# Kernel tuning notes

Hardware: AMD Instinct MI355X
Metric: run time of the kernel (lower is better)

The kernel has to match this reference:

```python
import jax, jax.numpy as jnp
import numpy as np

B = 4      # cfg.TRAIN.IMS_PER_BATCH
P = 256    # proposals per image (equal per image; all labels > 0)
C = 151    # cfg.MODEL.NUM_CLASSES
R = 51     # cfg.MODEL.NUM_RELATIONS
W = 0.5    # cfg.REL_INFER.NONE_BGREL_WEIGHT


def setup_inputs() -> dict:
    key = jax.random.key(0)
    k1, k2, k3, k4 = jax.random.split(key, 4)
    roi_scores = jax.random.normal(k1, (B * P, C), dtype=jnp.float32)
    rel_scores = jax.random.normal(k2, (B * P * P, R), dtype=jnp.float32)
    roi_labels = jax.random.randint(k3, (B * P,), 1, C, dtype=jnp.int32)  # labels > 0 (fg only)
    # sparse relation co-occurrence matrix densified; background relation slice set to 1
    relationship_mat = (jax.random.uniform(k4, (C, C, R)) < 0.05).astype(jnp.float32)
    relationship_mat = relationship_mat.at[:, :, 0].set(1.0)
    return {
        "roi_scores": roi_scores,
        "rel_scores": rel_scores,
        "relationship_mat": relationship_mat,
        "roi_labels": roi_labels,
        "num_images": B,
    }


def reference(roi_scores, rel_scores, relationship_mat, roi_labels, num_images):
    nb = num_images
    p = roi_scores.shape[0] // nb
    rel = rel_scores.reshape(nb, p, p, -1)          # [B, P, P, R]
    labels = roi_labels.reshape(nb, p)              # [B, P]
    # computed in the original forward but unused by the returned loss
    _unary = jax.nn.log_softmax(roi_scores, axis=1)
    off_diag = (1.0 - jnp.eye(p, dtype=roi_scores.dtype))  # zero out p == q pairs

    def per_image(lab, rl):
        # lab: [P] int, rl: [P, P, R]
        A = relationship_mat[lab]        # [P, C, R]  rows gathered by subject label
        At = relationship_mat[:, lab]    # [C, P, R]  cols gathered by subject label
        # b[p,q,c] = A[p,c,0]*rl[p,q,0] + W * sum_{r>=1} A[p,c,r]*rl[p,q,r]
        b = A[:, None, :, 0] * rl[:, :, None, 0] \
            + W * jnp.einsum('pcr,pqr->pqc', A[..., 1:], rl[..., 1:])
        # t[p,q,c] = At[c,p,0]*rl[q,p,0] + W * sum_{r>=1} At[c,p,r]*rl[q,p,r]
        t = At[..., 0].T[:, None, :] * rl[..., 0].T[:, :, None] \
            + W * jnp.einsum('cpr,qpr->pqc', At[..., 1:], rl[..., 1:])
        theta = 0.5 * (b + t) * off_diag[:, :, None]  # mask diagonal pairs
        theta = theta.sum(0)                          # sum over partner p -> [P, C]
        logp = jax.nn.log_softmax(theta, axis=1)
        return -logp[jnp.arange(p), lab]              # [P]

    loss = jax.vmap(per_image)(labels, rel)           # [B, P]
    return loss.mean()
```

## Files before the change

kernel.cpp:

```cpp
#include <hip/hip_runtime.h>
#include <math.h>

#define NB 4
#define PP 256
#define CC 151
#define RR 51
#define CM 160
#define KI 64
#define KS 64
#define NROW (NB*PP)
#define RELTOT (NB*PP*PP*RR)
#define ALIM (RELTOT - 8)
#define MLB 10240

typedef _Float16 half8 __attribute__((ext_vector_type(8)));
typedef float floatx16 __attribute__((ext_vector_type(16)));

#define OFF_M1 ((size_t)0)
#define OFF_M2 (OFF_M1 + (size_t)CC*MLB*2)
#define OFF_PT (OFF_M2 + (size_t)CC*MLB*2)

__global__ __launch_bounds__(256) void prep_kernel(const float* __restrict__ M,
                                                   _Float16* __restrict__ m1,
                                                   _Float16* __restrict__ m2,
                                                   float* __restrict__ out) {
    const int l = blockIdx.x;
    const int mat = blockIdx.y;
    if (l == 0 && mat == 0 && threadIdx.x == 0) *out = 0.f;
    _Float16* dst = (mat ? m2 : m1) + (size_t)l * MLB;
    for (int e = threadIdx.x; e < MLB; e += 256) {
        int oct = e / 1280;
        int rem = e - oct * 1280;
        int c = rem >> 3, j = rem & 7;
        int r = oct * 8 + j;
        float v = 0.f;
        if (r < RR && c < CC) {
            size_t src = ((size_t)(mat ? c * CC + l : l * CC + c)) * RR + r;
            v = (r == 0 ? 0.5f : 0.25f) * M[src];
        }
        dst[e] = (_Float16)v;
    }
}

__global__ __launch_bounds__(256) void gemm_kernel(const float* __restrict__ rel,
                                                   const _Float16* __restrict__ m1,
                                                   const _Float16* __restrict__ m2,
                                                   const int* __restrict__ labels,
                                                   float* __restrict__ part) {
    __shared__ _Float16 Bt[2][2560];
    const int tid  = threadIdx.x;
    const int ks   = blockIdx.x & 63;
    const int rbk  = (blockIdx.x >> 6) & 1;
    const int n    = blockIdx.x >> 7;
    const int wave = tid >> 6, lane = tid & 63;
    const int m32  = lane & 31, kh = lane >> 5;
    const int i0   = ks * 4;
    const int rowimg = rbk * 128 + wave * 32 + m32;

    int labs[4];
    #pragma unroll
    for (int j = 0; j < 4; ++j) labs[j] = labels[n * PP + i0 + j];

    floatx16 acc[5];
    #pragma unroll
    for (int ct = 0; ct < 5; ++ct)
        #pragma unroll
        for (int r2 = 0; r2 < 16; ++r2) acc[ct][r2] = 0.f;

    auto stageB = [&](int h, int buf) {
        const int il = h >> 3, mh = (h >> 2) & 1, t = h & 3;
        const _Float16* base = (mh ? m2 : m1) + (size_t)labs[il] * MLB + t * 2560;
        #pragma unroll
        for (int j = 0; j < 2; ++j) {
            int s = j * 256 + tid;
            if (s < 320) {
                __builtin_amdgcn_global_load_lds(
                    (const __attribute__((address_space(1))) unsigned int*)(base + s * 8),
                    (__attribute__((address_space(3))) unsigned int*)(&Bt[buf][(size_t)s * 8]),
                    16, 0, 0);
            }
        }
    };
    auto loadA = [&](int h, float* v) {
        const int il = h >> 3, mh = (h >> 2) & 1, t = h & 3;
        const int i = i0 + il;
        const int r0 = t * 16 + kh * 8;
        int idx = mh ? ((n * PP + rowimg) * PP + i) * RR + r0
                     : ((n * PP + i) * PP + rowimg) * RR + r0;
        idx = min(idx, ALIM);
        const float* p = rel + idx;
        #pragma unroll
        for (int j = 0; j < 8; ++j) v[j] = p[j];
    };

    stageB(0, 0);
    float av[8];
    loadA(0, av);

    #pragma unroll 2
    for (int h = 0; h < 32; ++h) {
        __syncthreads();
        if (h < 31) stageB(h + 1, (h + 1) & 1);
        float avn[8];
        if (h < 31) loadA(h + 1, avn);

        const bool dz = (i0 + (h >> 3)) == rowimg;
        half8 a;
        #pragma unroll
        for (int j = 0; j < 8; ++j) a[j] = (_Float16)(dz ? 0.f : av[j]);

        const _Float16* bb = &Bt[h & 1][(size_t)(kh * 160 + m32) * 8];
        #pragma unroll
        for (int ct = 0; ct < 5; ++ct) {
            half8 b = *(const half8*)(bb + ct * 256);
            acc[ct] = __builtin_amdgcn_mfma_f32_32x32x16_f16(a, b, acc[ct], 0, 0, 0);
        }
        #pragma unroll
        for (int j = 0; j < 8; ++j) av[j] = avn[j];
    }

    float* pb = part + ((size_t)ks * NROW + n * PP + rbk * 128 + wave * 32) * CM;
    #pragma unroll
    for (int ct = 0; ct < 5; ++ct)
        #pragma unroll
        for (int reg = 0; reg < 16; ++reg) {
            int row = (reg & 3) + 8 * (reg >> 2) + 4 * kh;
            pb[(size_t)row * CM + ct * 32 + m32] = acc[ct][reg];
        }
}

__global__ __launch_bounds__(256) void reduce_loss_kernel(const float* __restrict__ part,
                                                          const int* __restrict__ labels,
                                                          float* __restrict__ out) {
    __shared__ float th[CM];
    const int row = blockIdx.x;
    const int t = threadIdx.x;
    if (t < CM) {
        float s = 0.f;
        #pragma unroll
        for (int ks = 0; ks < KS; ++ks)
            s += part[((size_t)ks * NROW + row) * CM + t];
        th[t] = s;
    }
    __syncthreads();
    if (t < 64) {
        float v0 = (t < CC)       ? th[t]       : -INFINITY;
        float v1 = (t + 64 < CC)  ? th[t + 64]  : -INFINITY;
        float v2 = (t + 128 < CC) ? th[t + 128] : -INFINITY;
        float m = fmaxf(v0, fmaxf(v1, v2));
        #pragma unroll
        for (int o = 32; o > 0; o >>= 1) m = fmaxf(m, __shfl_xor(m, o, 64));
        float s = 0.f;
        if (t < CC)       s += expf(v0 - m);
        if (t + 64 < CC)  s += expf(v1 - m);
        if (t + 128 < CC) s += expf(v2 - m);
        #pragma unroll
        for (int o = 32; o > 0; o >>= 1) s += __shfl_xor(s, o, 64);
        if (t == 0) {
            atomicAdd(out, (m + logf(s) - th[labels[row]]) * (1.0f / NROW));
        }
    }
}

extern "C" void kernel_launch(void* const* d_in, const int* in_sizes, int n_in,
                              void* d_out, int out_size, void* d_ws, size_t ws_size,
                              hipStream_t stream) {
    const float* rel    = (const float*)d_in[1];
    const float* relmat = (const float*)d_in[2];
    const int*   labels = (const int*)d_in[3];
    float* out = (float*)d_out;
    char* ws = (char*)d_ws;

    _Float16* m1 = (_Float16*)(ws + OFF_M1);
    _Float16* m2 = (_Float16*)(ws + OFF_M2);
    float*  part = (float*)(ws + OFF_PT);

    prep_kernel<<<dim3(CC, 2), 256, 0, stream>>>(relmat, m1, m2, out);
    gemm_kernel<<<NB * 2 * KS, 256, 0, stream>>>(rel, m1, m2, labels, part);
    reduce_loss_kernel<<<NROW, 256, 0, stream>>>(part, labels, out);
}
```

Measured before the change: 166.0 us.

## Fuse prep, GEMM and loss reduction into one cooperative kernel with grid syncs

Merges the three launches (relation-matrix prep, MFMA GEMM, per-row log-softmax reduction) into one cooperative kernel of 512 blocks, separated by two grid-wide barriers. This removes two kernel launch gaps and their inter-kernel idle time. The reduction phase now has each block handle two rows instead of one block per row, which cuts its parallelism. Grid syncs add their own cost, and the cooperative launch needs all 512 blocks to be co-resident.

```diff
diff --git a/kernel.cpp b/kernel.cpp
--- a/kernel.cpp
+++ b/kernel.cpp
@@ -1,5 +1,8 @@
 #include <hip/hip_runtime.h>
+#include <hip/hip_cooperative_groups.h>
 #include <math.h>
+
+namespace cg = cooperative_groups;
 
 #define NB 4
 #define PP 256
@@ -12,6 +15,8 @@
 #define RELTOT (NB*PP*PP*RR)
 #define ALIM (RELTOT - 8)
 #define MLB 10240
+#define GRID 512
+#define NTHR (GRID*256)
 
 typedef _Float16 half8 __attribute__((ext_vector_type(8)));
 typedef float floatx16 __attribute__((ext_vector_type(16)));
@@ -20,144 +25,152 @@
 #define OFF_M2 (OFF_M1 + (size_t)CC*MLB*2)
 #define OFF_PT (OFF_M2 + (size_t)CC*MLB*2)
 
-__global__ __launch_bounds__(256) void prep_kernel(const float* __restrict__ M,
-                                                   _Float16* __restrict__ m1,
-                                                   _Float16* __restrict__ m2,
-                                                   float* __restrict__ out) {
-    const int l = blockIdx.x;
-    const int mat = blockIdx.y;
-    if (l == 0 && mat == 0 && threadIdx.x == 0) *out = 0.f;
-    _Float16* dst = (mat ? m2 : m1) + (size_t)l * MLB;
-    for (int e = threadIdx.x; e < MLB; e += 256) {
-        int oct = e / 1280;
-        int rem = e - oct * 1280;
-        int c = rem >> 3, j = rem & 7;
-        int r = oct * 8 + j;
+__global__ __launch_bounds__(256, 2)
+void fused_kernel(const float* __restrict__ rel,
+                  const float* __restrict__ M,
+                  const int* __restrict__ labels,
+                  float* __restrict__ out,
+                  _Float16* __restrict__ m1,
+                  _Float16* __restrict__ m2,
+                  float* __restrict__ part) {
+    __shared__ _Float16 Bt[2][2560];
+    const int tid = threadIdx.x;
+    const unsigned gtid = blockIdx.x * 256u + tid;
+
+    if (gtid == 0) atomicExch(out, 0.f);
+    for (unsigned e = gtid; e < 2u * CC * MLB; e += NTHR) {
+        unsigned mat = e / (CC * MLB);
+        unsigned e2  = e - mat * (CC * MLB);
+        unsigned l   = e2 / MLB;
+        unsigned rem = e2 - l * MLB;
+        unsigned oct = rem / 1280;
+        unsigned rm  = rem - oct * 1280;
+        unsigned c = rm >> 3, j = rm & 7;
+        unsigned r = oct * 8 + j;
         float v = 0.f;
         if (r < RR && c < CC) {
             size_t src = ((size_t)(mat ? c * CC + l : l * CC + c)) * RR + r;
             v = (r == 0 ? 0.5f : 0.25f) * M[src];
         }
-        dst[e] = (_Float16)v;
-    }
-}
-
-__global__ __launch_bounds__(256) void gemm_kernel(const float* __restrict__ rel,
-                                                   const _Float16* __restrict__ m1,
-                                                   const _Float16* __restrict__ m2,
-                                                   const int* __restrict__ labels,
-                                                   float* __restrict__ part) {
-    __shared__ _Float16 Bt[2][2560];
-    const int tid  = threadIdx.x;
-    const int ks   = blockIdx.x & 63;
-    const int rbk  = (blockIdx.x >> 6) & 1;
-    const int n    = blockIdx.x >> 7;
-    const int wave = tid >> 6, lane = tid & 63;
-    const int m32  = lane & 31, kh = lane >> 5;
-    const int i0   = ks * 4;
-    const int rowimg = rbk * 128 + wave * 32 + m32;
-
-    int labs[4];
-    #pragma unroll
-    for (int j = 0; j < 4; ++j) labs[j] = labels[n * PP + i0 + j];
-
-    floatx16 acc[5];
-    #pragma unroll
-    for (int ct = 0; ct < 5; ++ct)
-        #pragma unroll
-        for (int r2 = 0; r2 < 16; ++r2) acc[ct][r2] = 0.f;
-
-    auto stageB = [&](int h, int buf) {
-        const int il = h >> 3, mh = (h >> 2) & 1, t = h & 3;
-        const _Float16* base = (mh ? m2 : m1) + (size_t)labs[il] * MLB + t * 2560;
-        #pragma unroll
-        for (int j = 0; j < 2; ++j) {
-            int s = j * 256 + tid;
-            if (s < 320) {
-                __builtin_amdgcn_global_load_lds(
-                    (const __attribute__((address_space(1))) unsigned int*)(base + s * 8),
-                    (__attribute__((address_space(3))) unsigned int*)(&Bt[buf][(size_t)s * 8]),
-                    16, 0, 0);
-            }
-        }
-    };
-    auto loadA = [&](int h, float* v) {
-        const int il = h >> 3, mh = (h >> 2) & 1, t = h & 3;
-        const int i = i0 + il;
-        const int r0 = t * 16 + kh * 8;
-        int idx = mh ? ((n * PP + rowimg) * PP + i) * RR + r0
-                     : ((n * PP + i) * PP + rowimg) * RR + r0;
-        idx = min(idx, ALIM);
-        const float* p = rel + idx;
-        #pragma unroll
-        for (int j = 0; j < 8; ++j) v[j] = p[j];
-    };
-
-    stageB(0, 0);
-    float av[8];
-    loadA(0, av);
-
-    #pragma unroll 2
-    for (int h = 0; h < 32; ++h) {
-        __syncthreads();
-        if (h < 31) stageB(h + 1, (h + 1) & 1);
-        float avn[8];
-        if (h < 31) loadA(h + 1, avn);
-
-        const bool dz = (i0 + (h >> 3)) == rowimg;
-        half8 a;
-        #pragma unroll
-        for (int j = 0; j < 8; ++j) a[j] = (_Float16)(dz ? 0.f : av[j]);
-
-        const _Float16* bb = &Bt[h & 1][(size_t)(kh * 160 + m32) * 8];
-        #pragma unroll
-        for (int ct = 0; ct < 5; ++ct) {
-            half8 b = *(const half8*)(bb + ct * 256);
-            acc[ct] = __builtin_amdgcn_mfma_f32_32x32x16_f16(a, b, acc[ct], 0, 0, 0);
-        }
-        #pragma unroll
-        for (int j = 0; j < 8; ++j) av[j] = avn[j];
+        (mat ? m2 : m1)[(size_t)l * MLB + rem] = (_Float16)v;
     }
 
-    float* pb = part + ((size_t)ks * NROW + n * PP + rbk * 128 + wave * 32) * CM;
-    #pragma unroll
-    for (int ct = 0; ct < 5; ++ct)
+    cg::this_grid().sync();
+
+    {
+        const int ks   = blockIdx.x & 63;
+        const int rbk  = (blockIdx.x >> 6) & 1;
+        const int n    = blockIdx.x >> 7;
+        const int wave = tid >> 6, lane = tid & 63;
+        const int m32  = lane & 31, kh = lane >> 5;
+        const int i0   = ks * 4;
+        const int rowimg = rbk * 128 + wave * 32 + m32;
+
+        int labs[4];
         #pragma unroll
-        for (int reg = 0; reg < 16; ++reg) {
-            int row = (reg & 3) + 8 * (reg >> 2) + 4 * kh;
-            pb[(size_t)row * CM + ct * 32 + m32] = acc[ct][reg];
+        for (int j = 0; j < 4; ++j) labs[j] = labels[n * PP + i0 + j];
+
+        floatx16 acc[5];
+        #pragma unroll
+        for (int ct = 0; ct < 5; ++ct)
+            #pragma unroll
+            for (int r2 = 0; r2 < 16; ++r2) acc[ct][r2] = 0.f;
+
+        auto stageB = [&](int h, int buf) {
+            const int il = h >> 3, mh = (h >> 2) & 1, t = h & 3;
+            const _Float16* base = (mh ? m2 : m1) + (size_t)labs[il] * MLB + t * 2560;
+            #pragma unroll
+            for (int j = 0; j < 2; ++j) {
+                int s = j * 256 + tid;
+                if (s < 320) {
+                    __builtin_amdgcn_global_load_lds(
+                        (const __attribute__((address_space(1))) unsigned int*)(base + s * 8),
+                        (__attribute__((address_space(3))) unsigned int*)(&Bt[buf][(size_t)s * 8]),
+                        16, 0, 0);
+                }
+            }
+        };
+        auto loadA = [&](int h, float* v) {
+            const int il = h >> 3, mh = (h >> 2) & 1, t = h & 3;
+            const int i = i0 + il;
+            const int r0 = t * 16 + kh * 8;
+            int idx = mh ? ((n * PP + rowimg) * PP + i) * RR + r0
+                         : ((n * PP + i) * PP + rowimg) * RR + r0;
+            idx = min(idx, ALIM);
+            const float* p = rel + idx;
+            #pragma unroll
+            for (int j = 0; j < 8; ++j) v[j] = p[j];
+        };
+
+        stageB(0, 0);
+        float av[8];
+        loadA(0, av);
+
+        #pragma unroll 2
+        for (int h = 0; h < 32; ++h) {
+            __syncthreads();
+            if (h < 31) stageB(h + 1, (h + 1) & 1);
+            float avn[8];
+            if (h < 31) loadA(h + 1, avn);
+
+            const bool dz = (i0 + (h >> 3)) == rowimg;
+            half8 a;
+            #pragma unroll
+            for (int j = 0; j < 8; ++j) a[j] = (_Float16)(dz ? 0.f : av[j]);
+
+            const _Float16* bb = &Bt[h & 1][(size_t)(kh * 160 + m32) * 8];
+            #pragma unroll
+            for (int ct = 0; ct < 5; ++ct) {
+                half8 b = *(const half8*)(bb + ct * 256);
+                acc[ct] = __builtin_amdgcn_mfma_f32_32x32x16_f16(a, b, acc[ct], 0, 0, 0);
+            }
+            #pragma unroll
+            for (int j = 0; j < 8; ++j) av[j] = avn[j];
         }
-}
 
-__global__ __launch_bounds__(256) void reduce_loss_kernel(const float* __restrict__ part,
-                                                          const int* __restrict__ labels,
-                                                          float* __restrict__ out) {
-    __shared__ float th[CM];
-    const int row = blockIdx.x;
-    const int t = threadIdx.x;
-    if (t < CM) {
-        float s = 0.f;
+        float* pb = part + ((size_t)ks * NROW + n * PP + rbk * 128 + wave * 32) * CM;
         #pragma unroll
-        for (int ks = 0; ks < KS; ++ks)
-            s += part[((size_t)ks * NROW + row) * CM + t];
-        th[t] = s;
+        for (int ct = 0; ct < 5; ++ct)
+            #pragma unroll
+            for (int reg = 0; reg < 16; ++reg) {
+                int row = (reg & 3) + 8 * (reg >> 2) + 4 * kh;
+                pb[(size_t)row * CM + ct * 32 + m32] = acc[ct][reg];
+            }
     }
-    __syncthreads();
-    if (t < 64) {
-        float v0 = (t < CC)       ? th[t]       : -INFINITY;
-        float v1 = (t + 64 < CC)  ? th[t + 64]  : -INFINITY;
-        float v2 = (t + 128 < CC) ? th[t + 128] : -INFINITY;
-        float m = fmaxf(v0, fmaxf(v1, v2));
+
+    cg::this_grid().sync();
+
+    {
+        float* th = (float*)Bt;
         #pragma unroll
-        for (int o = 32; o > 0; o >>= 1) m = fmaxf(m, __shfl_xor(m, o, 64));
-        float s = 0.f;
-        if (t < CC)       s += expf(v0 - m);
-        if (t + 64 < CC)  s += expf(v1 - m);
-        if (t + 128 < CC) s += expf(v2 - m);
-        #pragma unroll
-        for (int o = 32; o > 0; o >>= 1) s += __shfl_xor(s, o, 64);
-        if (t == 0) {
-            atomicAdd(out, (m + logf(s) - th[labels[row]]) * (1.0f / NROW));
+        for (int sub = 0; sub < 2; ++sub) {
+            const int row = blockIdx.x * 2 + sub;
+            const int t = tid;
+            if (t < CM) {
+                float s = 0.f;
+                #pragma unroll
+                for (int ks = 0; ks < KS; ++ks)
+                    s += part[((size_t)ks * NROW + row) * CM + t];
+                th[t] = s;
+            }
+            __syncthreads();
+            if (t < 64) {
+                float v0 = (t < CC)       ? th[t]       : -INFINITY;
+                float v1 = (t + 64 < CC)  ? th[t + 64]  : -INFINITY;
+                float v2 = (t + 128 < CC) ? th[t + 128] : -INFINITY;
+                float m = fmaxf(v0, fmaxf(v1, v2));
+                #pragma unroll
+                for (int o = 32; o > 0; o >>= 1) m = fmaxf(m, __shfl_xor(m, o, 64));
+                float s = 0.f;
+                if (t < CC)       s += expf(v0 - m);
+                if (t + 64 < CC)  s += expf(v1 - m);
+                if (t + 128 < CC) s += expf(v2 - m);
+                #pragma unroll
+                for (int o = 32; o > 0; o >>= 1) s += __shfl_xor(s, o, 64);
+                if (t == 0)
+                    atomicAdd(out, (m + logf(s) - th[labels[row]]) * (1.0f / NROW));
+            }
+            __syncthreads();
         }
     }
 }
@@ -175,7 +188,8 @@
     _Float16* m2 = (_Float16*)(ws + OFF_M2);
     float*  part = (float*)(ws + OFF_PT);
 
-    prep_kernel<<<dim3(CC, 2), 256, 0, stream>>>(relmat, m1, m2, out);
-    gemm_kernel<<<NB * 2 * KS, 256, 0, stream>>>(rel, m1, m2, labels, part);
-    reduce_loss_kernel<<<NROW, 256, 0, stream>>>(part, labels, out);
+    void* args[] = {(void*)&rel, (void*)&relmat, (void*)&labels, (void*)&out,
+                    (void*)&m1, (void*)&m2, (void*)&part};
+    hipLaunchCooperativeKernel((const void*)fused_kernel, dim3(GRID), dim3(256),
+                               args, 0, stream);
 }
```

Result: slower. 280.1 us (+68.8%).

## Merge m1/m2 halves per iteration and deepen LDS pipeline to triple buffering

Applied to the files above, without the earlier changes.

Each loop iteration now stages both the m1 and m2 tiles for the same partner/k-chunk and issues two MFMAs per column tile, halving the iteration count and the number of barriers. B tiles are now triple-buffered with a two-step lookahead, and A loads fetch both the direct and transposed rel rows together. This raises LDS use and register pressure (launch_bounds min-blocks set to 2) in exchange for fewer synchronisations and more memory-level parallelism.

```diff
diff --git a/kernel.cpp b/kernel.cpp
--- a/kernel.cpp
+++ b/kernel.cpp
@@ -6,12 +6,12 @@
 #define CC 151
 #define RR 51
 #define CM 160
-#define KI 64
 #define KS 64
 #define NROW (NB*PP)
 #define RELTOT (NB*PP*PP*RR)
 #define ALIM (RELTOT - 8)
 #define MLB 10240
+#define TILE 5120
 
 typedef _Float16 half8 __attribute__((ext_vector_type(8)));
 typedef float floatx16 __attribute__((ext_vector_type(16)));
@@ -42,12 +42,12 @@
     }
 }
 
-__global__ __launch_bounds__(256) void gemm_kernel(const float* __restrict__ rel,
-                                                   const _Float16* __restrict__ m1,
-                                                   const _Float16* __restrict__ m2,
-                                                   const int* __restrict__ labels,
-                                                   float* __restrict__ part) {
-    __shared__ _Float16 Bt[2][2560];
+__global__ __launch_bounds__(256, 2) void gemm_kernel(const float* __restrict__ rel,
+                                                      const _Float16* __restrict__ m1,
+                                                      const _Float16* __restrict__ m2,
+                                                      const int* __restrict__ labels,
+                                                      float* __restrict__ part) {
+    __shared__ _Float16 Bt[3][TILE];
     const int tid  = threadIdx.x;
     const int ks   = blockIdx.x & 63;
     const int rbk  = (blockIdx.x >> 6) & 1;
@@ -68,55 +68,66 @@
         for (int r2 = 0; r2 < 16; ++r2) acc[ct][r2] = 0.f;
 
     auto stageB = [&](int h, int buf) {
-        const int il = h >> 3, mh = (h >> 2) & 1, t = h & 3;
-        const _Float16* base = (mh ? m2 : m1) + (size_t)labs[il] * MLB + t * 2560;
+        const int il = h >> 2, t = h & 3;
+        const size_t moff = (size_t)labs[il] * MLB + t * 2560;
+        const _Float16* b1 = m1 + moff;
+        const _Float16* b2 = m2 + moff;
         #pragma unroll
-        for (int j = 0; j < 2; ++j) {
+        for (int j = 0; j < 3; ++j) {
             int s = j * 256 + tid;
-            if (s < 320) {
+            if (s < 640) {
+                const _Float16* g = (s < 320) ? b1 + (size_t)s * 8
+                                              : b2 + (size_t)(s - 320) * 8;
                 __builtin_amdgcn_global_load_lds(
-                    (const __attribute__((address_space(1))) unsigned int*)(base + s * 8),
+                    (const __attribute__((address_space(1))) unsigned int*)g,
                     (__attribute__((address_space(3))) unsigned int*)(&Bt[buf][(size_t)s * 8]),
                     16, 0, 0);
             }
         }
     };
     auto loadA = [&](int h, float* v) {
-        const int il = h >> 3, mh = (h >> 2) & 1, t = h & 3;
+        const int il = h >> 2, t = h & 3;
         const int i = i0 + il;
         const int r0 = t * 16 + kh * 8;
-        int idx = mh ? ((n * PP + rowimg) * PP + i) * RR + r0
-                     : ((n * PP + i) * PP + rowimg) * RR + r0;
-        idx = min(idx, ALIM);
-        const float* p = rel + idx;
+        int idx0 = ((n * PP + i) * PP + rowimg) * RR + r0;
+        int idx1 = ((n * PP + rowimg) * PP + i) * RR + r0;
+        idx0 = min(idx0, ALIM);
+        idx1 = min(idx1, ALIM);
+        const float* p0 = rel + idx0;
+        const float* p1 = rel + idx1;
         #pragma unroll
-        for (int j = 0; j < 8; ++j) v[j] = p[j];
+        for (int j = 0; j < 8; ++j) { v[j] = p0[j]; v[8 + j] = p1[j]; }
     };
 
     stageB(0, 0);
-    float av[8];
+    stageB(1, 1);
+    float av[16];
     loadA(0, av);
 
-    #pragma unroll 2
-    for (int h = 0; h < 32; ++h) {
+    for (int h = 0; h < 16; ++h) {
         __syncthreads();
-        if (h < 31) stageB(h + 1, (h + 1) & 1);
-        float avn[8];
-        if (h < 31) loadA(h + 1, avn);
+        if (h < 14) stageB(h + 2, (h + 2) % 3);
+        float avn[16];
+        if (h < 15) loadA(h + 1, avn);
 
-        const bool dz = (i0 + (h >> 3)) == rowimg;
-        half8 a;
+        const bool dz = (i0 + (h >> 2)) == rowimg;
+        half8 a0, a1;
         #pragma unroll
-        for (int j = 0; j < 8; ++j) a[j] = (_Float16)(dz ? 0.f : av[j]);
+        for (int j = 0; j < 8; ++j) {
+            a0[j] = (_Float16)(dz ? 0.f : av[j]);
+            a1[j] = (_Float16)(dz ? 0.f : av[8 + j]);
+        }
 
-        const _Float16* bb = &Bt[h & 1][(size_t)(kh * 160 + m32) * 8];
+        const _Float16* bb = &Bt[h % 3][(size_t)(kh * 160 + m32) * 8];
         #pragma unroll
         for (int ct = 0; ct < 5; ++ct) {
-            half8 b = *(const half8*)(bb + ct * 256);
-            acc[ct] = __builtin_amdgcn_mfma_f32_32x32x16_f16(a, b, acc[ct], 0, 0, 0);
+            half8 b0 = *(const half8*)(bb + ct * 256);
+            half8 b1 = *(const half8*)(bb + 2560 + ct * 256);
+            acc[ct] = __builtin_amdgcn_mfma_f32_32x32x16_f16(a0, b0, acc[ct], 0, 0, 0);
+            acc[ct] = __builtin_amdgcn_mfma_f32_32x32x16_f16(a1, b1, acc[ct], 0, 0, 0);
         }
         #pragma unroll
-        for (int j = 0; j < 8; ++j) av[j] = avn[j];
+        for (int j = 0; j < 16; ++j) av[j] = avn[j];
     }
 
     float* pb = part + ((size_t)ks * NROW + n * PP + rbk * 128 + wave * 32) * CM;
```

Result: slower. 169.4 us (+2.1%).

## Split GEMM K-loop across two wave groups and reduce partials in LDS

Applied to the files above, without the earlier changes.

The GEMM block grows to 512 threads: one group of four waves handles the m1 (subject) half of the reduction and the other handles the m2 (transposed) half, each with its own double-buffered LDS tile. This halves the serial K-loop per wave (16 steps instead of 32) and increases in-flight memory parallelism. At the end, group 1 writes its accumulators to LDS and group 0 adds them before storing, which adds extra barriers and LDS traffic in the epilogue and raises per-block resource use.

```diff
diff --git a/kernel.cpp b/kernel.cpp
--- a/kernel.cpp
+++ b/kernel.cpp
@@ -6,7 +6,6 @@
 #define CC 151
 #define RR 51
 #define CM 160
-#define KI 64
 #define KS 64
 #define NROW (NB*PP)
 #define RELTOT (NB*PP*PP*RR)
@@ -42,25 +41,31 @@
     }
 }
 
-__global__ __launch_bounds__(256) void gemm_kernel(const float* __restrict__ rel,
-                                                   const _Float16* __restrict__ m1,
-                                                   const _Float16* __restrict__ m2,
-                                                   const int* __restrict__ labels,
-                                                   float* __restrict__ part) {
-    __shared__ _Float16 Bt[2][2560];
+__global__ __launch_bounds__(512, 4) void gemm_kernel(const float* __restrict__ rel,
+                                                      const _Float16* __restrict__ m1,
+                                                      const _Float16* __restrict__ m2,
+                                                      const int* __restrict__ labels,
+                                                      float* __restrict__ part) {
+    __shared__ _Float16 Bt[2][2][2560];
     const int tid  = threadIdx.x;
     const int ks   = blockIdx.x & 63;
     const int rbk  = (blockIdx.x >> 6) & 1;
     const int n    = blockIdx.x >> 7;
-    const int wave = tid >> 6, lane = tid & 63;
+    const int wave = tid >> 6;
+    const int grp  = wave >> 2;
+    const int wg   = wave & 3;
+    const int lane = tid & 63;
     const int m32  = lane & 31, kh = lane >> 5;
+    const int gtid = tid & 255;
     const int i0   = ks * 4;
-    const int rowimg = rbk * 128 + wave * 32 + m32;
+    const int rowimg = rbk * 128 + wg * 32 + m32;
 
     int labs[4];
     #pragma unroll
     for (int j = 0; j < 4; ++j) labs[j] = labels[n * PP + i0 + j];
 
+    const _Float16* mbase = grp ? m2 : m1;
+
     floatx16 acc[5];
     #pragma unroll
     for (int ct = 0; ct < 5; ++ct)
@@ -68,25 +73,26 @@
         for (int r2 = 0; r2 < 16; ++r2) acc[ct][r2] = 0.f;
 
     auto stageB = [&](int h, int buf) {
-        const int il = h >> 3, mh = (h >> 2) & 1, t = h & 3;
-        const _Float16* base = (mh ? m2 : m1) + (size_t)labs[il] * MLB + t * 2560;
-        #pragma unroll
-        for (int j = 0; j < 2; ++j) {
-            int s = j * 256 + tid;
-            if (s < 320) {
-                __builtin_amdgcn_global_load_lds(
-                    (const __attribute__((address_space(1))) unsigned int*)(base + s * 8),
-                    (__attribute__((address_space(3))) unsigned int*)(&Bt[buf][(size_t)s * 8]),
-                    16, 0, 0);
-            }
+        const int il = h >> 2, t = h & 3;
+        const _Float16* base = mbase + (size_t)labs[il] * MLB + t * 2560;
+        __builtin_amdgcn_global_load_lds(
+            (const __attribute__((address_space(1))) unsigned int*)(base + (size_t)gtid * 8),
+            (__attribute__((address_space(3))) unsigned int*)(&Bt[grp][buf][(size_t)gtid * 8]),
+            16, 0, 0);
+        if (gtid < 64) {
+            int s = 256 + gtid;
+            __builtin_amdgcn_global_load_lds(
+                (const __attribute__((address_space(1))) unsigned int*)(base + (size_t)s * 8),
+                (__attribute__((address_space(3))) unsigned int*)(&Bt[grp][buf][(size_t)s * 8]),
+                16, 0, 0);
         }
     };
     auto loadA = [&](int h, float* v) {
-        const int il = h >> 3, mh = (h >> 2) & 1, t = h & 3;
+        const int il = h >> 2, t = h & 3;
         const int i = i0 + il;
         const int r0 = t * 16 + kh * 8;
-        int idx = mh ? ((n * PP + rowimg) * PP + i) * RR + r0
-                     : ((n * PP + i) * PP + rowimg) * RR + r0;
+        int idx = grp ? ((n * PP + rowimg) * PP + i) * RR + r0
+                      : ((n * PP + i) * PP + rowimg) * RR + r0;
         idx = min(idx, ALIM);
         const float* p = rel + idx;
         #pragma unroll
@@ -97,19 +103,18 @@
     float av[8];
     loadA(0, av);
 
-    #pragma unroll 2
-    for (int h = 0; h < 32; ++h) {
+    for (int h = 0; h < 16; ++h) {
         __syncthreads();
-        if (h < 31) stageB(h + 1, (h + 1) & 1);
+        if (h < 15) stageB(h + 1, (h + 1) & 1);
         float avn[8];
-        if (h < 31) loadA(h + 1, avn);
-
-        const bool dz = (i0 + (h >> 3)) == rowimg;
+        if (h < 15) loadA(h + 1, avn);
+
+        const bool dz = (i0 + (h >> 2)) == rowimg;
         half8 a;
         #pragma unroll
         for (int j = 0; j < 8; ++j) a[j] = (_Float16)(dz ? 0.f : av[j]);
 
-        const _Float16* bb = &Bt[h & 1][(size_t)(kh * 160 + m32) * 8];
+        const _Float16* bb = &Bt[grp][h & 1][(size_t)(kh * 160 + m32) * 8];
         #pragma unroll
         for (int ct = 0; ct < 5; ++ct) {
             half8 b = *(const half8*)(bb + ct * 256);
@@ -119,14 +124,29 @@
         for (int j = 0; j < 8; ++j) av[j] = avn[j];
     }
 
-    float* pb = part + ((size_t)ks * NROW + n * PP + rbk * 128 + wave * 32) * CM;
+    float* ep = (float*)Bt;
+    float* pb = part + ((size_t)ks * NROW + n * PP + rbk * 128) * CM;
     #pragma unroll
-    for (int ct = 0; ct < 5; ++ct)
-        #pragma unroll
-        for (int reg = 0; reg < 16; ++reg) {
-            int row = (reg & 3) + 8 * (reg >> 2) + 4 * kh;
-            pb[(size_t)row * CM + ct * 32 + m32] = acc[ct][reg];
-        }
+    for (int ct = 0; ct < 5; ++ct) {
+        __syncthreads();
+        if (grp == 1) {
+            #pragma unroll
+            for (int reg = 0; reg < 16; ++reg) {
+                int rowD = (reg & 3) + 8 * (reg >> 2) + 4 * kh;
+                ep[(size_t)(wg * 32 + rowD) * 32 + m32] = acc[ct][reg];
+            }
+        }
+        __syncthreads();
+        if (grp == 0) {
+            #pragma unroll
+            for (int reg = 0; reg < 16; ++reg) {
+                int rowD = (reg & 3) + 8 * (reg >> 2) + 4 * kh;
+                int rloc = wg * 32 + rowD;
+                pb[(size_t)rloc * CM + ct * 32 + m32] =
+                    acc[ct][reg] + ep[(size_t)rloc * 32 + m32];
+            }
+        }
+    }
 }
 
 __global__ __launch_bounds__(256) void reduce_loss_kernel(const float* __restrict__ part,
@@ -176,6 +196,6 @@
     float*  part = (float*)(ws + OFF_PT);
 
     prep_kernel<<<dim3(CC, 2), 256, 0, stream>>>(relmat, m1, m2, out);
-    gemm_kernel<<<NB * 2 * KS, 256, 0, stream>>>(rel, m1, m2, labels, part);
+    gemm_kernel<<<NB * 2 * KS, 512, 0, stream>>>(rel, m1, m2, labels, part);
     reduce_loss_kernel<<<NROW, 256, 0, stream>>>(part, labels, out);
 }
```

New measurement: 172.2 us. 3.8% more time.
